# Kernel optimization log

Measured on AMD Instinct MI355X. Metric: run time of the kernel, lower is better.

Reference implementation:

```python
import jax, jax.numpy as jnp
import numpy as np
import math

T, B, I, H, L = 1024, 64, 512, 512, 2


def setup_inputs() -> dict:
    key = jax.random.key(0)
    ks = jax.random.split(key, 16)
    s = 1.0 / math.sqrt(H)
    inp = {
        "x": jax.random.normal(ks[0], (T, B, I), jnp.float32),
        "h0": jax.random.normal(ks[1], (L, B, H), jnp.float32),
        "c0": jax.random.normal(ks[2], (L, B, H), jnp.float32),
    }
    names = ["w_ih_0", "w_hh_0", "b_ih_0", "b_hh_0", "w_ih_1", "w_hh_1", "b_ih_1", "b_hh_1"]
    shapes = [(4 * H, I), (4 * H, H), (4 * H,), (4 * H,), (4 * H, H), (4 * H, H), (4 * H,), (4 * H,)]
    for i, (n, sh) in enumerate(zip(names, shapes)):
        inp[n] = jax.random.normal(ks[3 + i], sh, jnp.float32) * s
    return inp


def _lstm_layer(x, h0, c0, w_ih, w_hh, b_ih, b_hh):
    # x: [T,B,in]; h0,c0: [B,H].  NOTE: original module re-reads the INITIAL
    # (h0,c0) at every timestep (no temporal recurrence), so this vectorizes over T.
    hh = h0 @ w_hh.T + b_hh                          # [B,4H], same for all t
    gates = jnp.einsum('tbi,gi->tbg', x, w_ih) + b_ih + hh[None]  # [T,B,4H]
    i_g, f_g, g_g, o_g = jnp.split(gates, 4, axis=-1)
    cy = jax.nn.sigmoid(f_g) * c0[None] + jax.nn.sigmoid(i_g) * jnp.tanh(g_g)
    hy = jax.nn.sigmoid(o_g) * jnp.tanh(cy)
    return hy, cy                                     # [T,B,H] each


def reference(x, h0, c0, w_ih_0, w_hh_0, b_ih_0, b_hh_0, w_ih_1, w_hh_1, b_ih_1, b_hh_1):
    params = [(w_ih_0, w_hh_0, b_ih_0, b_hh_0), (w_ih_1, w_hh_1, b_ih_1, b_hh_1)]
    cur = x
    last_h, last_c = [], []
    for l in range(L):
        hy, cy = _lstm_layer(cur, h0[l], c0[l], *params[l])
        last_h.append(hy[-1])
        last_c.append(cy[-1])
        cur = hy
    t, b, h = cur.shape
    result = cur.reshape(t * b, 1, h)  # == torch.cat over time then unsqueeze(1)
    return result, jnp.stack(last_h), jnp.stack(last_c)
```

## Files before the change

kernel.cpp:

```cpp
#include <hip/hip_runtime.h>
#include <hip/hip_bf16.h>

#define T_DIM 1024
#define B_DIM 64
#define H_DIM 512

typedef __attribute__((ext_vector_type(8))) short short8;
typedef __attribute__((ext_vector_type(4))) float f32x4;

typedef __attribute__((address_space(3))) void lds_void_t;
typedef __attribute__((address_space(1))) void glob_void_t;

static __device__ __forceinline__ unsigned short f2b_rne(float f) {
  unsigned u = __float_as_uint(f);
  u += 0x7fffu + ((u >> 16) & 1u);
  return (unsigned short)(u >> 16);
}

static __device__ __forceinline__ float sigm(float x) {
  return 1.0f / (1.0f + __expf(-x));
}
static __device__ __forceinline__ float tanh_fast(float x) {
  float e = __expf(2.0f * fabsf(x));
  float t = 1.0f - 2.0f / (e + 1.0f);
  return copysignf(t, x);
}

__global__ void conv_f2b(const float* __restrict__ in,
                         unsigned short* __restrict__ out, int n4) {
  int idx = blockIdx.x * blockDim.x + threadIdx.x;
  int stride = gridDim.x * blockDim.x;
  for (int i = idx; i < n4; i += stride) {
    float4 v = reinterpret_cast<const float4*>(in)[i];
    ushort4 o;
    o.x = f2b_rne(v.x); o.y = f2b_rne(v.y);
    o.z = f2b_rne(v.z); o.w = f2b_rne(v.w);
    reinterpret_cast<ushort4*>(out)[i] = o;
  }
}

__global__ void hh_bias(const float* __restrict__ h0,
                        const float* __restrict__ whh0, const float* __restrict__ whh1,
                        const float* __restrict__ bih0, const float* __restrict__ bhh0,
                        const float* __restrict__ bih1, const float* __restrict__ bhh1,
                        float* __restrict__ hhb) {
  int g = blockIdx.x * blockDim.x + threadIdx.x;
  int b = blockIdx.y;
  int l = blockIdx.z;
  const float* wh = l ? whh1 : whh0;
  const float* bi = l ? bih1 : bih0;
  const float* bh = l ? bhh1 : bhh0;
  const float4* hr = reinterpret_cast<const float4*>(h0 + ((size_t)l * B_DIM + b) * H_DIM);
  const float4* wr = reinterpret_cast<const float4*>(wh + (size_t)g * H_DIM);
  float acc = bi[g] + bh[g];
#pragma unroll 4
  for (int k = 0; k < H_DIM / 4; ++k) {
    float4 a = hr[k], w = wr[k];
    acc += a.x * w.x + a.y * w.y + a.z * w.z + a.w * w.w;
  }
  hhb[((size_t)l * B_DIM + b) * 2048 + g] = acc;
}

template <int LAYER>
__global__ __launch_bounds__(256, 2) void lstm_gemm(
    const unsigned short* __restrict__ Abf,
    const unsigned short* __restrict__ Wbf,
    const float* __restrict__ hhb,
    const float* __restrict__ c0l,
    unsigned short* __restrict__ hy_bf,
    float* __restrict__ out_hy,
    float* __restrict__ out_lasth,
    float* __restrict__ out_lastc) {
  __shared__ __attribute__((aligned(16))) unsigned short Alds[128 * 64];
  __shared__ __attribute__((aligned(16))) unsigned short Blds[128 * 64];

  const int tid = threadIdx.x;
  const int lane = tid & 63;
  const int wid = tid >> 6;
  const int bh = blockIdx.x;
  const int bm = blockIdx.y;
  const int m0 = bm * 128;
  const int h0 = bh * 32;
  const int lane_lo = lane & 15, lane_hi = lane >> 4;
  const int srow = tid >> 3;
  const int slot = tid & 7;

  f32x4 acc[2][8] = {};

  for (int ks = 0; ks < 8; ++ks) {
    const int k0 = ks * 64;
#pragma unroll
    for (int i = 0; i < 4; ++i) {
      int row = i * 32 + srow;
      int sch = slot ^ (row & 7);
      const unsigned short* src = Abf + (size_t)(m0 + row) * 512 + k0 + sch * 8;
      char* dst = (char*)Alds + i * 4096 + wid * 1024;
      __builtin_amdgcn_global_load_lds((const glob_void_t*)src, (lds_void_t*)dst, 16, 0, 0);
    }
#pragma unroll
    for (int i = 0; i < 4; ++i) {
      int n = i * 32 + srow;
      int sch = slot ^ (n & 7);
      int wrow = (n >> 5) * H_DIM + h0 + (n & 31);
      const unsigned short* src = Wbf + (size_t)wrow * 512 + k0 + sch * 8;
      char* dst = (char*)Blds + i * 4096 + wid * 1024;
      __builtin_amdgcn_global_load_lds((const glob_void_t*)src, (lds_void_t*)dst, 16, 0, 0);
    }
    __syncthreads();

#pragma unroll
    for (int kk = 0; kk < 2; ++kk) {
      const int cbase = kk * 4 + lane_hi;
      short8 aF[2];
#pragma unroll
      for (int r = 0; r < 2; ++r) {
        int row = wid * 32 + r * 16 + lane_lo;
        aF[r] = *reinterpret_cast<const short8*>(
            (const char*)Alds + row * 128 + ((cbase ^ (row & 7)) << 4));
      }
      short8 bF[8];
#pragma unroll
      for (int c = 0; c < 8; ++c) {
        int n = c * 16 + lane_lo;
        bF[c] = *reinterpret_cast<const short8*>(
            (const char*)Blds + n * 128 + ((cbase ^ (n & 7)) << 4));
      }
#pragma unroll
      for (int r = 0; r < 2; ++r)
#pragma unroll
        for (int c = 0; c < 8; ++c)
          acc[r][c] = __builtin_amdgcn_mfma_f32_16x16x32_bf16(aF[r], bF[c], acc[r][c], 0, 0, 0);
    }
    __syncthreads();
  }

#pragma unroll
  for (int r = 0; r < 2; ++r) {
#pragma unroll
    for (int j = 0; j < 4; ++j) {
      int m = m0 + wid * 32 + r * 16 + lane_hi * 4 + j;
      int b = m & (B_DIM - 1);
      bool isLast = (m >> 6) == (T_DIM - 1);
      const float* hb = hhb + (size_t)b * 2048;
#pragma unroll
      for (int hc = 0; hc < 2; ++hc) {
        int h = h0 + hc * 16 + lane_lo;
        float gi = acc[r][0 + hc][j] + hb[h];
        float gf = acc[r][2 + hc][j] + hb[512 + h];
        float gg = acc[r][4 + hc][j] + hb[1024 + h];
        float go = acc[r][6 + hc][j] + hb[1536 + h];
        float iv = sigm(gi), fv = sigm(gf), gv = tanh_fast(gg), ov = sigm(go);
        float cv = fv * c0l[b * H_DIM + h] + iv * gv;
        float hv = ov * tanh_fast(cv);
        if (LAYER == 0) {
          hy_bf[(size_t)m * H_DIM + h] = f2b_rne(hv);
        } else {
          out_hy[(size_t)m * H_DIM + h] = hv;
        }
        if (isLast) {
          out_lasth[b * H_DIM + h] = hv;
          out_lastc[b * H_DIM + h] = cv;
        }
      }
    }
  }
}

extern "C" void kernel_launch(void* const* d_in, const int* in_sizes, int n_in,
                              void* d_out, int out_size, void* d_ws, size_t ws_size,
                              hipStream_t stream) {
  const float* x    = (const float*)d_in[0];
  const float* h0   = (const float*)d_in[1];
  const float* c0   = (const float*)d_in[2];
  const float* wih0 = (const float*)d_in[3];
  const float* whh0 = (const float*)d_in[4];
  const float* bih0 = (const float*)d_in[5];
  const float* bhh0 = (const float*)d_in[6];
  const float* wih1 = (const float*)d_in[7];
  const float* whh1 = (const float*)d_in[8];
  const float* bih1 = (const float*)d_in[9];
  const float* bhh1 = (const float*)d_in[10];
  float* out = (float*)d_out;

  char* ws = (char*)d_ws;
  unsigned short* x_bf   = (unsigned short*)(ws);
  unsigned short* hy0_bf = (unsigned short*)(ws + 67108864);
  unsigned short* w0_bf  = (unsigned short*)(ws + 134217728);
  unsigned short* w1_bf  = (unsigned short*)(ws + 136314880);
  float*          hhb    = (float*)(ws + 138412032);

  conv_f2b<<<2048, 256, 0, stream>>>(x, x_bf, 33554432 / 4);
  conv_f2b<<<512, 256, 0, stream>>>(wih0, w0_bf, 1048576 / 4);
  conv_f2b<<<512, 256, 0, stream>>>(wih1, w1_bf, 1048576 / 4);
  hh_bias<<<dim3(8, 64, 2), 256, 0, stream>>>(h0, whh0, whh1, bih0, bhh0, bih1, bhh1, hhb);

  float* res   = out;
  float* lasth = out + 33554432;
  float* lastc = out + 33554432 + 65536;

  lstm_gemm<0><<<dim3(16, 512), 256, 0, stream>>>(
      x_bf, w0_bf, hhb, c0, hy0_bf, nullptr, lasth, lastc);
  lstm_gemm<1><<<dim3(16, 512), 256, 0, stream>>>(
      hy0_bf, w1_bf, hhb + 64 * 2048, c0 + 64 * 512, nullptr, res,
      lasth + 64 * 512, lastc + 64 * 512);
}
```

Measured before the change: 778.0 us.

## Use 2x2 wave tiling, XCD-aware block swizzle, and wave-per-row hh_bias

The GEMM wave layout changes from 4x1 (each wave 32 rows by all 128 columns) to 2x2 (each wave 64 rows by 64 columns), so each wave loads 4 A and 4 B fragments per k-step instead of 2 and 8. This cuts LDS fragment reads per MFMA. The 1D grid is remapped so blocks that share M rows land on the same XCD, which should improve L2 reuse. hh_bias now assigns one wave per gate row and reduces with shuffles across the batch, which gives coalesced weight loads.

```diff
diff --git a/kernel.cpp b/kernel.cpp
--- a/kernel.cpp
+++ b/kernel.cpp
@@ -44,21 +44,28 @@
                         const float* __restrict__ bih0, const float* __restrict__ bhh0,
                         const float* __restrict__ bih1, const float* __restrict__ bhh1,
                         float* __restrict__ hhb) {
-  int g = blockIdx.x * blockDim.x + threadIdx.x;
-  int b = blockIdx.y;
-  int l = blockIdx.z;
+  const int l = blockIdx.y;
+  const int wid = threadIdx.x >> 6;
+  const int lane = threadIdx.x & 63;
+  const int g = blockIdx.x * 4 + wid;
   const float* wh = l ? whh1 : whh0;
   const float* bi = l ? bih1 : bih0;
   const float* bh = l ? bhh1 : bhh0;
-  const float4* hr = reinterpret_cast<const float4*>(h0 + ((size_t)l * B_DIM + b) * H_DIM);
   const float4* wr = reinterpret_cast<const float4*>(wh + (size_t)g * H_DIM);
-  float acc = bi[g] + bh[g];
-#pragma unroll 4
-  for (int k = 0; k < H_DIM / 4; ++k) {
-    float4 a = hr[k], w = wr[k];
-    acc += a.x * w.x + a.y * w.y + a.z * w.z + a.w * w.w;
-  }
-  hhb[((size_t)l * B_DIM + b) * 2048 + g] = acc;
+  float4 w0 = wr[lane * 2];
+  float4 w1 = wr[lane * 2 + 1];
+  float bias = bi[g] + bh[g];
+  const float* h0l = h0 + (size_t)l * B_DIM * H_DIM;
+  for (int b = 0; b < B_DIM; ++b) {
+    const float4* hr = reinterpret_cast<const float4*>(h0l + (size_t)b * H_DIM);
+    float4 a0 = hr[lane * 2];
+    float4 a1 = hr[lane * 2 + 1];
+    float acc = a0.x * w0.x + a0.y * w0.y + a0.z * w0.z + a0.w * w0.w +
+                a1.x * w1.x + a1.y * w1.y + a1.z * w1.z + a1.w * w1.w;
+#pragma unroll
+    for (int off = 32; off; off >>= 1) acc += __shfl_xor(acc, off);
+    if (lane == 0) hhb[((size_t)l * B_DIM + b) * 2048 + g] = acc + bias;
+  }
 }
 
 template <int LAYER>
@@ -77,15 +84,19 @@
   const int tid = threadIdx.x;
   const int lane = tid & 63;
   const int wid = tid >> 6;
-  const int bh = blockIdx.x;
-  const int bm = blockIdx.y;
+  const int wr = wid >> 1, wc = wid & 1;
+
+  const int lin = blockIdx.x;
+  const int wg = (lin & 7) * 1024 + (lin >> 3);
+  const int bh = wg & 15;
+  const int bm = wg >> 4;
   const int m0 = bm * 128;
-  const int h0 = bh * 32;
+  const int h0v = bh * 32;
   const int lane_lo = lane & 15, lane_hi = lane >> 4;
   const int srow = tid >> 3;
   const int slot = tid & 7;
 
-  f32x4 acc[2][8] = {};
+  f32x4 acc[4][4] = {};
 
   for (int ks = 0; ks < 8; ++ks) {
     const int k0 = ks * 64;
@@ -101,7 +112,7 @@
     for (int i = 0; i < 4; ++i) {
       int n = i * 32 + srow;
       int sch = slot ^ (n & 7);
-      int wrow = (n >> 5) * H_DIM + h0 + (n & 31);
+      int wrow = (n >> 5) * H_DIM + h0v + (n & 31);
       const unsigned short* src = Wbf + (size_t)wrow * 512 + k0 + sch * 8;
       char* dst = (char*)Blds + i * 4096 + wid * 1024;
       __builtin_amdgcn_global_load_lds((const glob_void_t*)src, (lds_void_t*)dst, 16, 0, 0);
@@ -111,56 +122,53 @@
 #pragma unroll
     for (int kk = 0; kk < 2; ++kk) {
       const int cbase = kk * 4 + lane_hi;
-      short8 aF[2];
-#pragma unroll
-      for (int r = 0; r < 2; ++r) {
-        int row = wid * 32 + r * 16 + lane_lo;
+      short8 aF[4];
+#pragma unroll
+      for (int r = 0; r < 4; ++r) {
+        int row = wr * 64 + r * 16 + lane_lo;
         aF[r] = *reinterpret_cast<const short8*>(
             (const char*)Alds + row * 128 + ((cbase ^ (row & 7)) << 4));
       }
-      short8 bF[8];
-#pragma unroll
-      for (int c = 0; c < 8; ++c) {
-        int n = c * 16 + lane_lo;
-        bF[c] = *reinterpret_cast<const short8*>(
+      short8 bF[4];
+#pragma unroll
+      for (int g = 0; g < 4; ++g) {
+        int n = g * 32 + wc * 16 + lane_lo;
+        bF[g] = *reinterpret_cast<const short8*>(
             (const char*)Blds + n * 128 + ((cbase ^ (n & 7)) << 4));
       }
 #pragma unroll
-      for (int r = 0; r < 2; ++r)
-#pragma unroll
-        for (int c = 0; c < 8; ++c)
-          acc[r][c] = __builtin_amdgcn_mfma_f32_16x16x32_bf16(aF[r], bF[c], acc[r][c], 0, 0, 0);
+      for (int r = 0; r < 4; ++r)
+#pragma unroll
+        for (int g = 0; g < 4; ++g)
+          acc[r][g] = __builtin_amdgcn_mfma_f32_16x16x32_bf16(aF[r], bF[g], acc[r][g], 0, 0, 0);
     }
     __syncthreads();
   }
 
-#pragma unroll
-  for (int r = 0; r < 2; ++r) {
+  const int h = h0v + wc * 16 + lane_lo;
+#pragma unroll
+  for (int r = 0; r < 4; ++r) {
 #pragma unroll
     for (int j = 0; j < 4; ++j) {
-      int m = m0 + wid * 32 + r * 16 + lane_hi * 4 + j;
+      int m = m0 + wr * 64 + r * 16 + lane_hi * 4 + j;
       int b = m & (B_DIM - 1);
       bool isLast = (m >> 6) == (T_DIM - 1);
       const float* hb = hhb + (size_t)b * 2048;
-#pragma unroll
-      for (int hc = 0; hc < 2; ++hc) {
-        int h = h0 + hc * 16 + lane_lo;
-        float gi = acc[r][0 + hc][j] + hb[h];
-        float gf = acc[r][2 + hc][j] + hb[512 + h];
-        float gg = acc[r][4 + hc][j] + hb[1024 + h];
-        float go = acc[r][6 + hc][j] + hb[1536 + h];
-        float iv = sigm(gi), fv = sigm(gf), gv = tanh_fast(gg), ov = sigm(go);
-        float cv = fv * c0l[b * H_DIM + h] + iv * gv;
-        float hv = ov * tanh_fast(cv);
-        if (LAYER == 0) {
-          hy_bf[(size_t)m * H_DIM + h] = f2b_rne(hv);
-        } else {
-          out_hy[(size_t)m * H_DIM + h] = hv;
-        }
-        if (isLast) {
-          out_lasth[b * H_DIM + h] = hv;
-          out_lastc[b * H_DIM + h] = cv;
-        }
+      float gi = acc[r][0][j] + hb[h];
+      float gf = acc[r][1][j] + hb[512 + h];
+      float gg = acc[r][2][j] + hb[1024 + h];
+      float go = acc[r][3][j] + hb[1536 + h];
+      float iv = sigm(gi), fv = sigm(gf), gv = tanh_fast(gg), ov = sigm(go);
+      float cv = fv * c0l[b * H_DIM + h] + iv * gv;
+      float hv = ov * tanh_fast(cv);
+      if (LAYER == 0) {
+        hy_bf[(size_t)m * H_DIM + h] = f2b_rne(hv);
+      } else {
+        out_hy[(size_t)m * H_DIM + h] = hv;
+      }
+      if (isLast) {
+        out_lasth[b * H_DIM + h] = hv;
+        out_lastc[b * H_DIM + h] = cv;
       }
     }
   }
@@ -192,15 +200,15 @@
   conv_f2b<<<2048, 256, 0, stream>>>(x, x_bf, 33554432 / 4);
   conv_f2b<<<512, 256, 0, stream>>>(wih0, w0_bf, 1048576 / 4);
   conv_f2b<<<512, 256, 0, stream>>>(wih1, w1_bf, 1048576 / 4);
-  hh_bias<<<dim3(8, 64, 2), 256, 0, stream>>>(h0, whh0, whh1, bih0, bhh0, bih1, bhh1, hhb);
+  hh_bias<<<dim3(512, 2), 256, 0, stream>>>(h0, whh0, whh1, bih0, bhh0, bih1, bhh1, hhb);
 
   float* res   = out;
   float* lasth = out + 33554432;
   float* lastc = out + 33554432 + 65536;
 
-  lstm_gemm<0><<<dim3(16, 512), 256, 0, stream>>>(
+  lstm_gemm<0><<<8192, 256, 0, stream>>>(
       x_bf, w0_bf, hhb, c0, hy0_bf, nullptr, lasth, lastc);
-  lstm_gemm<1><<<dim3(16, 512), 256, 0, stream>>>(
+  lstm_gemm<1><<<8192, 256, 0, stream>>>(
       hy0_bf, w1_bf, hhb + 64 * 2048, c0 + 64 * 512, nullptr, res,
       lasth + 64 * 512, lastc + 64 * 512);
 }
```

Measured after the change: 674.9 us. 1.15x faster.
